# Kernel optimization log

Measured on AMD Instinct MI355X. Metric: run time of the kernel, lower is better.

## Reference

```python
import jax, jax.numpy as jnp
import numpy as np

N = 32768   # nodes
E = 32768   # edges
ND, ED, GD = 12, 5, 11
H = 64
T = 4
STEPS = 3


def setup_inputs() -> dict:
    key = jax.random.key(0)
    ks = jax.random.split(key, 24)
    s = 0.05
    p = lambda k, sh: (jax.random.normal(k, sh) * s).astype(jnp.float32)
    return dict(
        x=jax.random.normal(ks[0], (N, ND), jnp.float32),
        edge_index=jax.random.randint(ks[1], (2, E), 0, N, jnp.int64),
        edge_attr=jax.random.uniform(ks[2], (E, ED), jnp.float32),
        u=jax.random.normal(ks[3], (1, GD), jnp.float32),
        Wp=p(ks[4], (H, ND + GD)), bp=p(ks[5], (H,)),
        We1=p(ks[6], (H, ED)), be1=p(ks[7], (H,)),
        We2=p(ks[8], (H * H, H)), be2=p(ks[9], (H * H,)),
        root=p(ks[10], (H, H)), conv_b=p(ks[11], (H,)),
        Wih=p(ks[12], (3 * H, H)), bih=p(ks[13], (3 * H,)),
        Whh=p(ks[14], (3 * H, H)), bhh=p(ks[15], (3 * H,)),
        Wd1=p(ks[16], (H, 2 * H + ED)), bd1=p(ks[17], (H,)),
        Wd2=p(ks[18], (H // 2, H)), bd2=p(ks[19], (H // 2,)),
        Wd3=p(ks[20], (T, H // 2)), bd3=p(ks[21], (T,)),
    )


def _forward(x, edge_index, edge_attr, u,
             Wp, bp, We1, be1, We2, be2, root, conv_b,
             Wih, bih, Whh, bhh, Wd1, bd1, Wd2, bd2, Wd3, bd3):
    n = x.shape[0]
    e = edge_attr.shape[0]
    src, dst = edge_index[0], edge_index[1]

    # input projection with broadcast global features (batch=None path)
    u_node = jnp.broadcast_to(u, (n, u.shape[-1]))
    h = jnp.tanh(jnp.concatenate([x, u_node], axis=-1) @ Wp.T + bp)

    # edge MLP -> per-edge (H,H) weight matrices; edge_attr is loop-invariant
    ew = jax.nn.relu(edge_attr @ We1.T + be1) @ We2.T + be2   # (E, H*H)
    ew = ew.reshape(e, H, H)                                   # (E, H, H)

    # mean-aggregation denominators (clamped to 1 like scatter-mean)
    counts = jnp.clip(jax.ops.segment_sum(jnp.ones((e,), h.dtype), dst, num_segments=n), 1.0)

    for _ in range(STEPS):
        # NNConv: gather src features, per-edge matmul, scatter-mean into dst
        msg = jnp.einsum('eh,eho->eo', h[src], ew)             # (E, H)
        agg = jax.ops.segment_sum(msg, dst, num_segments=n) / counts[:, None]
        m = jax.nn.relu(agg + h @ root + conv_b)               # dropout off (eval)
        # GRUCell (torch gate order: r, z, n)
        gi = m @ Wih.T + bih
        gh = h @ Whh.T + bhh
        r = jax.nn.sigmoid(gi[:, :H] + gh[:, :H])
        z = jax.nn.sigmoid(gi[:, H:2 * H] + gh[:, H:2 * H])
        ng = jnp.tanh(gi[:, 2 * H:] + r * gh[:, 2 * H:])
        h = (1.0 - z) * ng + z * h

    # per-edge decoder
    e_in = jnp.concatenate([h[src], h[dst], edge_attr], axis=-1)
    d = jax.nn.relu(e_in @ Wd1.T + bd1)
    d = jax.nn.relu(d @ Wd2.T + bd2)
    return d @ Wd3.T + bd3                                     # (E, T)


def reference(x, edge_index, edge_attr, u,
              Wp, bp, We1, be1, We2, be2, root, conv_b,
              Wih, bih, Whh, bhh, Wd1, bd1, Wd2, bd2, Wd3, bd3):
    return _forward(x, edge_index, edge_attr, u,
                    Wp, bp, We1, be1, We2, be2, root, conv_b,
                    Wih, bih, Whh, bhh, Wd1, bd1, Wd2, bd2, Wd3, bd3)
```

## Files before the change

kernel.cpp:

```cpp
#include <hip/hip_runtime.h>
#include <hip/hip_bf16.h>
#include <stdint.h>


#define N_NODES 32768
#define N_EDGES 32768
#define STEPS 3

typedef __attribute__((ext_vector_type(8))) short short8;
typedef __attribute__((ext_vector_type(4))) float float4v;

__device__ __forceinline__ float bf2f(unsigned short u) {
    union { unsigned int i; float f; } v; v.i = ((unsigned int)u) << 16; return v.f;
}
__device__ __forceinline__ unsigned short f2bf(float f) {
    union { float f; unsigned int i; } v; v.f = f;
    unsigned int x = v.i;
    return (unsigned short)((x + 0x7fffu + ((x >> 16) & 1u)) >> 16);
}

__device__ __forceinline__ void gload_lds16(const void* g, void* l) {
    __builtin_amdgcn_global_load_lds(
        (__attribute__((address_space(1))) void*)g,
        (__attribute__((address_space(3))) void*)l, 16, 0, 0);
}

__global__ __launch_bounds__(256) void k_setup(
    const float* __restrict__ root, const float* __restrict__ Wih,
    const float* __restrict__ Whh,
    const float* __restrict__ We2, const float* __restrict__ be2,
    const float* __restrict__ Wd1, const float* __restrict__ bd1,
    const float* __restrict__ Wd2,
    const float* __restrict__ x, const float* __restrict__ u,
    const float* __restrict__ Wp, const float* __restrict__ bp,
    const float* __restrict__ ea, const float* __restrict__ We1,
    const float* __restrict__ be1,
    unsigned short* __restrict__ rootTf, unsigned short* __restrict__ wcombf,
    unsigned short* __restrict__ w2tf,
    unsigned short* __restrict__ wd1f, unsigned short* __restrict__ wd2f,
    unsigned short* __restrict__ hb,
    unsigned short* __restrict__ hidT, float* __restrict__ cnts)
{
    int b = blockIdx.x, tid = threadIdx.x;
    if (b < 144) {
        int i = b * 256 + tid;
        if (i < 4096) {
            int j = i & 7, lane = (i >> 3) & 63, g = i >> 9;
            int kb = g >> 2, nf = g & 3;
            int o = nf * 16 + (lane & 15);
            int k = kb * 32 + (lane >> 4) * 8 + j;
            rootTf[i] = f2bf(root[k * 64 + o]);
        } else if (i < 4096 + 32768) {
            int t = i - 4096;
            int j = t & 7, lane = (t >> 3) & 63, g = t >> 9;
            int kb = g >> 4, nf = g & 15;
            int cp = nf * 16 + (lane & 15);
            int k = kb * 32 + (lane >> 4) * 8 + j;
            float v;
            if (cp < 128)      v = (k < 64) ? Wih[cp * 64 + k] : Whh[cp * 64 + (k - 64)];
            else if (cp < 192) v = (k < 64) ? Wih[cp * 64 + k] : 0.f;
            else               v = (k < 64) ? 0.f : Whh[(cp - 64) * 64 + (k - 64)];
            wcombf[t] = f2bf(v);
        }
    } else if (b < 1184) {
        int t = (b - 144) * 256 + tid;
        if (t < 65 * 4096) {
            int kk = t >> 12, r = t & 4095;
            int j = r & 7, lane = (r >> 3) & 63, g = r >> 9;
            int half = g >> 2, nf = g & 3;
            int o = nf * 16 + (lane & 15);
            int hh = half * 32 + (lane >> 4) * 8 + j;
            float v = (kk < 64) ? We2[((size_t)(hh * 64 + o)) * 64 + kk]
                                : be2[(size_t)hh * 64 + o];
            w2tf[t] = f2bf(v);
        }
    } else if (b < 1232) {
        int i = (b - 1184) * 256 + tid;
        if (i < 10240) {
            int j = i & 7, lane = (i >> 3) & 63, g = i >> 9;
            int kb = g >> 2, nf = g & 3;
            int o = nf * 16 + (lane & 15);
            int k = kb * 32 + (lane >> 4) * 8 + j;
            float v = (k < 133) ? Wd1[(size_t)o * 133 + k] : (k == 133 ? bd1[o] : 0.f);
            wd1f[i] = f2bf(v);
        } else if (i < 10240 + 2048) {
            int t = i - 10240;
            int j = t & 7, lane = (t >> 3) & 63, g = t >> 9;
            int kb = g >> 1, nf = g & 1;
            int o = nf * 16 + (lane & 15);
            int k = kb * 32 + (lane >> 4) * 8 + j;
            wd2f[t] = f2bf(Wd2[(size_t)o * 64 + k]);
        }
    } else if (b < 9424) {
        int idx = (b - 1232) * 256 + tid;
        int n = idx >> 6, j = idx & 63;
        const float* wr = Wp + j * 23;
        const float* xr = x + (size_t)n * 12;
        float s = bp[j];
#pragma unroll
        for (int i = 0; i < 12; i++) s += xr[i] * wr[i];
#pragma unroll
        for (int i = 0; i < 11; i++) s += u[i] * wr[12 + i];
        hb[idx] = f2bf(tanhf(s));
    } else if (b < 17616) {
        int idx = (b - 9424) * 256 + tid;
        int el = idx & 63, j = (idx >> 6) & 63, eb = idx >> 12;
        int e = eb * 64 + el;
        float s = be1[j];
#pragma unroll
        for (int i = 0; i < 5; i++) s += ea[(size_t)e * 5 + i] * We1[j * 5 + i];
        hidT[(size_t)j * N_EDGES + e] = f2bf(s > 0.f ? s : 0.f);
    } else {
        int idx = (b - 17616) * 1024 + tid * 4;
        if (idx < 32768) {
            float4v z = {0.f, 0.f, 0.f, 0.f};
            *(float4v*)(cnts + idx) = z;
        }
    }
}

__global__ __launch_bounds__(256) void k_counts(
    const int* __restrict__ ei, float* __restrict__ counts)
{
    int i = blockIdx.x * 256 + threadIdx.x;
    if (i < N_EDGES) atomicAdd(&counts[ei[N_EDGES + i]], 1.0f);
}

__global__ __launch_bounds__(1024) void k_scan(
    const float* __restrict__ cnts, int* __restrict__ off, int* __restrict__ woff)
{
    __shared__ int part[1024];
    int t = threadIdx.x;
    int loc[32];
    int s = 0;
#pragma unroll
    for (int i = 0; i < 32; i++) { loc[i] = s; s += (int)cnts[t * 32 + i]; }
    part[t] = s;
    __syncthreads();
    for (int d = 1; d < 1024; d <<= 1) {
        int y = (t >= d) ? part[t - d] : 0;
        __syncthreads();
        part[t] += y;
        __syncthreads();
    }
    int pre = (t == 0) ? 0 : part[t - 1];
#pragma unroll
    for (int i = 0; i < 32; i++) {
        off[t * 32 + i] = pre + loc[i];
        woff[t * 32 + i] = pre + loc[i];
    }
    if (t == 1023) off[32768] = part[1023];
}

__global__ __launch_bounds__(256) void k_scatter(
    const int* __restrict__ ei, int* __restrict__ woff, int* __restrict__ eorder)
{
    int e = blockIdx.x * 256 + threadIdx.x;
    if (e < N_EDGES) {
        int d = ei[N_EDGES + e];
        int slot = atomicAdd(&woff[d], 1);
        eorder[slot] = e;
    }
}

__global__ __launch_bounds__(512, 2) void k_msg_fused(
    const unsigned short* __restrict__ hidT,
    const unsigned short* __restrict__ hb,
    const unsigned short* __restrict__ w2tf,
    const int* __restrict__ ei,
    float* __restrict__ msgbuf)
{
    __shared__ __attribute__((aligned(16))) unsigned char smem[81920];
    unsigned short* stg = (unsigned short*)smem;
    unsigned short* hvl = (unsigned short*)(smem + 65536);
    float* red = (float*)smem;

    int tid = threadIdx.x, w = tid >> 6, lane = tid & 63;
    int l15 = lane & 15, quad = lane >> 4;
    int kg = w & 3, eg = w >> 2;
    int ebase = blockIdx.x * 128;
    int n_w = 16 + (kg == 3 ? 1 : 0);

#pragma unroll
    for (int i = 0; i < 8; i++) {
        int row = w * 8 + i;
        unsigned int v = *((const unsigned int*)(hidT + (size_t)row * N_EDGES + ebase) + lane);
        *((unsigned int*)hvl + row * 64 + lane) = v;
    }
    short8 afr[4][2];
#pragma unroll
    for (int t = 0; t < 4; t++) {
        int src = ei[ebase + eg * 64 + t * 16 + l15];
#pragma unroll
        for (int hh = 0; hh < 2; hh++)
            afr[t][hh] = *(const short8*)(hb + (size_t)src * 64 + hh * 32 + quad * 8);
    }

    auto stage = [&](int r, int db) {
        const unsigned short* g = w2tf + (size_t)(kg * 16 + r) * 4096;
        unsigned short* d = stg + (kg * 2 + db) * 4096;
#pragma unroll
        for (int c = 0; c < 4; c++) {
            int ch = eg * 4 + c;
            gload_lds16(g + ch * 512 + lane * 8, d + ch * 512);
        }
    };

    stage(0, 0);
    stage(1, 1);
    asm volatile("s_waitcnt lgkmcnt(0)" ::: "memory");
    __builtin_amdgcn_s_barrier();

    float4v acc[4][4] = {};
    for (int r = 0; r <= 16; r++) {
        int db = r & 1;
        if (r >= n_w - 1) { asm volatile("s_waitcnt vmcnt(0)" ::: "memory"); }
        else              { asm volatile("s_waitcnt vmcnt(4)" ::: "memory"); }
        __builtin_amdgcn_s_barrier();

        bool act = (r < n_w);
        short8 bfr[2][4];
        unsigned long long hu[4] = {0ull, 0ull, 0ull, 0ull};
        bool bias = (r == 16);
        if (act) {
            const unsigned short* bb = stg + (kg * 2 + db) * 4096;
#pragma unroll
            for (int hh = 0; hh < 2; hh++)
#pragma unroll
                for (int nf = 0; nf < 4; nf++)
                    bfr[hh][nf] = *(const short8*)(bb + (hh * 4 + nf) * 512 + lane * 8);
            if (!bias) {
#pragma unroll
                for (int t = 0; t < 4; t++)
                    hu[t] = *(const unsigned long long*)(hvl + (kg * 16 + r) * 128 + eg * 64 + t * 16 + quad * 4);
            }
        }
        asm volatile("s_waitcnt lgkmcnt(0)" ::: "memory");
        __builtin_amdgcn_s_barrier();
        if (r + 2 < n_w) stage(r + 2, db);

        if (act) {
#pragma unroll
            for (int t = 0; t < 4; t++) {
                float4v T[4];
#pragma unroll
                for (int nf = 0; nf < 4; nf++) {
                    float4v z = {0.f, 0.f, 0.f, 0.f};
                    T[nf] = __builtin_amdgcn_mfma_f32_16x16x32_bf16(afr[t][0], bfr[0][nf], z, 0, 0, 0);
                }
#pragma unroll
                for (int nf = 0; nf < 4; nf++)
                    T[nf] = __builtin_amdgcn_mfma_f32_16x16x32_bf16(afr[t][1], bfr[1][nf], T[nf], 0, 0, 0);
#pragma unroll
                for (int rr = 0; rr < 4; rr++) {
                    float hvv = bias ? 1.0f : bf2f((unsigned short)(hu[t] >> (16 * rr)));
#pragma unroll
                    for (int nf = 0; nf < 4; nf++)
                        acc[t][nf][rr] += hvv * T[nf][rr];
                }
            }
        }
    }

    int row_w = tid >> 2, kq = tid & 3;
#pragma unroll
    for (int nf = 0; nf < 4; nf++) {
        __syncthreads();
#pragma unroll
        for (int t = 0; t < 4; t++)
#pragma unroll
            for (int rr = 0; rr < 4; rr++)
                red[kg * 2304 + (eg * 64 + t * 16 + quad * 4 + rr) * 18 + l15] = acc[t][nf][rr];
        __syncthreads();
        float4v s = {0.f, 0.f, 0.f, 0.f};
#pragma unroll
        for (int g2 = 0; g2 < 4; g2++) {
            const float* rp = red + g2 * 2304 + row_w * 18 + kq * 4;
#pragma unroll
            for (int j = 0; j < 4; j++) s[j] += rp[j];
        }
        *(float4v*)(msgbuf + (size_t)(ebase + row_w) * 64 + nf * 16 + kq * 4) = s;
    }
}

__global__ __launch_bounds__(256) void k_node(
    const unsigned short* __restrict__ hb_in,
    const unsigned short* __restrict__ rootTf,
    const unsigned short* __restrict__ wcombf,
    const float* __restrict__ msgbuf, const int* __restrict__ off,
    const int* __restrict__ eorder,
    const float* __restrict__ counts,
    const float* __restrict__ conv_b,
    const float* __restrict__ bih, const float* __restrict__ bhh,
    unsigned short* __restrict__ hb_out)
{
    __shared__ unsigned short m_lds[64 * 72];
    __shared__ float aggl[64 * 68];
    int tid = threadIdx.x, w = tid >> 6, lane = tid & 63;
    int l15 = lane & 15, quad = lane >> 4;
    int node0 = blockIdx.x * 64;
    int row0 = w * 16;

    {
        int nl = tid >> 2, cg = tid & 3;
        int nn = node0 + nl;
        int s0 = off[nn], s1 = off[nn + 1];
        float acc[16] = {};
        for (int sl = s0; sl < s1; sl++) {
            int e = eorder[sl];
            const float* mr = msgbuf + (size_t)e * 64 + cg * 16;
#pragma unroll
            for (int q = 0; q < 4; q++) {
                float4v v = *(const float4v*)(mr + 4 * q);
#pragma unroll
                for (int j = 0; j < 4; j++) acc[4 * q + j] += v[j];
            }
        }
#pragma unroll
        for (int k = 0; k < 16; k++) aggl[nl * 68 + cg * 16 + k] = acc[k];
    }
    __syncthreads();

    float4v acc1[4] = {};
    {
        short8 a1[2];
#pragma unroll
        for (int kb = 0; kb < 2; kb++)
            a1[kb] = *(const short8*)(hb_in + (size_t)(node0 + row0 + l15) * 64 + kb * 32 + quad * 8);
#pragma unroll
        for (int kb = 0; kb < 2; kb++)
#pragma unroll
            for (int nf = 0; nf < 4; nf++) {
                short8 b = *(const short8*)(rootTf + (size_t)((kb * 4 + nf) * 64 + lane) * 8);
                acc1[nf] = __builtin_amdgcn_mfma_f32_16x16x32_bf16(a1[kb], b, acc1[nf], 0, 0, 0);
            }
    }
#pragma unroll
    for (int rr = 0; rr < 4; rr++) {
        int nl = row0 + quad * 4 + rr;
        float cnt = counts[node0 + nl]; if (cnt < 1.f) cnt = 1.f;
        float rcp = 1.f / cnt;
#pragma unroll
        for (int nf = 0; nf < 4; nf++) {
            int c = nf * 16 + l15;
            float av = aggl[nl * 68 + c];
            float mv = av * rcp + acc1[nf][rr] + conv_b[c];
            m_lds[nl * 72 + c] = f2bf(mv > 0.f ? mv : 0.f);
        }
    }
    __syncthreads();

    float4v acc2[16] = {};
#pragma unroll
    for (int kb = 0; kb < 4; kb++) {
        short8 a2;
        if (kb < 2)
            a2 = *(const short8*)(m_lds + (row0 + l15) * 72 + kb * 32 + quad * 8);
        else
            a2 = *(const short8*)(hb_in + (size_t)(node0 + row0 + l15) * 64 + (kb - 2) * 32 + quad * 8);
#pragma unroll
        for (int nf = 0; nf < 16; nf++) {
            short8 b = *(const short8*)(wcombf + (size_t)((kb * 16 + nf) * 64 + lane) * 8);
            acc2[nf] = __builtin_amdgcn_mfma_f32_16x16x32_bf16(a2, b, acc2[nf], 0, 0, 0);
        }
    }

#pragma unroll
    for (int nf0 = 0; nf0 < 4; nf0++) {
        int c = nf0 * 16 + l15;
        float br = bih[c] + bhh[c];
        float bz = bih[64 + c] + bhh[64 + c];
        float bni = bih[128 + c], bnh = bhh[128 + c];
#pragma unroll
        for (int rr = 0; rr < 4; rr++) {
            int node = node0 + row0 + quad * 4 + rr;
            float gr = 1.f / (1.f + __expf(-(acc2[nf0][rr] + br)));
            float gz = 1.f / (1.f + __expf(-(acc2[nf0 + 4][rr] + bz)));
            float ng = tanhf(acc2[nf0 + 8][rr] + bni + gr * (acc2[nf0 + 12][rr] + bnh));
            float ho = bf2f(hb_in[(size_t)node * 64 + c]);
            float hn = (1.f - gz) * ng + gz * ho;
            hb_out[(size_t)node * 64 + c] = f2bf(hn);
        }
    }
}

__global__ __launch_bounds__(256) void k_decoder(
    const unsigned short* __restrict__ hb, const int* __restrict__ ei,
    const float* __restrict__ ea,
    const unsigned short* __restrict__ wd1f, const unsigned short* __restrict__ wd2f,
    const float* __restrict__ bd2,
    const float* __restrict__ Wd3, const float* __restrict__ bd3,
    float* __restrict__ out)
{
    __shared__ unsigned short d1f[4][1024];
    __shared__ float d2s[4][16 * 33];
    int tid = threadIdx.x, w = tid >> 6, lane = tid & 63;
    int l15 = lane & 15, quad = lane >> 4;
    int ebase = blockIdx.x * 64 + w * 16;
    int e = ebase + l15;
    int src = ei[e], dst = ei[N_EDGES + e];

    short8 a[5];
#pragma unroll
    for (int kb = 0; kb < 2; kb++) {
        a[kb]     = *(const short8*)(hb + (size_t)src * 64 + kb * 32 + quad * 8);
        a[2 + kb] = *(const short8*)(hb + (size_t)dst * 64 + kb * 32 + quad * 8);
    }
    {
        union { short8 v; unsigned short u[8]; } tea;
#pragma unroll
        for (int j = 0; j < 8; j++) {
            float vv = 0.f;
            if (quad == 0) vv = (j < 5) ? ea[(size_t)e * 5 + j] : (j == 5 ? 1.f : 0.f);
            tea.u[j] = f2bf(vv);
        }
        a[4] = tea.v;
    }

    float4v acc1[4] = {};
#pragma unroll
    for (int kb = 0; kb < 5; kb++)
#pragma unroll
        for (int nf = 0; nf < 4; nf++) {
            short8 b = *(const short8*)(wd1f + (size_t)((kb * 4 + nf) * 64 + lane) * 8);
            acc1[nf] = __builtin_amdgcn_mfma_f32_16x16x32_bf16(a[kb], b, acc1[nf], 0, 0, 0);
        }
#pragma unroll
    for (int nf = 0; nf < 4; nf++) {
        int kbp = nf >> 1;
        int lanep_hi = ((nf & 1) * 2 + (l15 >> 3)) * 16;
        int jp = l15 & 7;
#pragma unroll
        for (int r = 0; r < 4; r++) {
            float v = acc1[nf][r];
            d1f[w][kbp * 512 + (lanep_hi + quad * 4 + r) * 8 + jp] = f2bf(v > 0.f ? v : 0.f);
        }
    }
    float4v acc2[2] = {};
#pragma unroll
    for (int kb = 0; kb < 2; kb++) {
        short8 a2 = *(const short8*)(&d1f[w][kb * 512 + lane * 8]);
#pragma unroll
        for (int nf = 0; nf < 2; nf++) {
            short8 b = *(const short8*)(wd2f + (size_t)((kb * 2 + nf) * 64 + lane) * 8);
            acc2[nf] = __builtin_amdgcn_mfma_f32_16x16x32_bf16(a2, b, acc2[nf], 0, 0, 0);
        }
    }
#pragma unroll
    for (int nf = 0; nf < 2; nf++) {
        int c = nf * 16 + l15;
        float bias = bd2[c];
#pragma unroll
        for (int r = 0; r < 4; r++) {
            float v = acc2[nf][r] + bias;
            d2s[w][(quad * 4 + r) * 33 + c] = v > 0.f ? v : 0.f;
        }
    }
    {
        int e_l = lane >> 2, t = lane & 3;
        float s = bd3[t];
        const float* w3 = Wd3 + t * 32;
        const float* dr = &d2s[w][e_l * 33];
#pragma unroll
        for (int k = 0; k < 32; k++) s += w3[k] * dr[k];
        out[(size_t)(ebase + e_l) * 4 + t] = s;
    }
}

extern "C" void kernel_launch(void* const* d_in, const int* in_sizes, int n_in,
                              void* d_out, int out_size, void* d_ws, size_t ws_size,
                              hipStream_t stream)
{
    const float* x      = (const float*)d_in[0];
    const int*   ei     = (const int*)d_in[1];
    const float* ea     = (const float*)d_in[2];
    const float* u      = (const float*)d_in[3];
    const float* Wp     = (const float*)d_in[4];
    const float* bp     = (const float*)d_in[5];
    const float* We1    = (const float*)d_in[6];
    const float* be1    = (const float*)d_in[7];
    const float* We2    = (const float*)d_in[8];
    const float* be2    = (const float*)d_in[9];
    const float* root   = (const float*)d_in[10];
    const float* conv_b = (const float*)d_in[11];
    const float* Wih    = (const float*)d_in[12];
    const float* bih    = (const float*)d_in[13];
    const float* Whh    = (const float*)d_in[14];
    const float* bhh    = (const float*)d_in[15];
    const float* Wd1    = (const float*)d_in[16];
    const float* bd1    = (const float*)d_in[17];
    const float* Wd2    = (const float*)d_in[18];
    const float* bd2    = (const float*)d_in[19];
    const float* Wd3    = (const float*)d_in[20];
    const float* bd3    = (const float*)d_in[21];
    float* out = (float*)d_out;

    char* ws = (char*)d_ws;
    size_t off_b = 0;
    auto take = [&](size_t bytes) -> char* {
        char* p = ws + off_b; off_b = (off_b + bytes + 255) & ~(size_t)255; return p;
    };
    unsigned short* hb     = (unsigned short*)take((size_t)N_NODES * 64 * 2);
    unsigned short* hidT   = (unsigned short*)take((size_t)N_EDGES * 64 * 2);
    float*          msgbuf = (float*)take((size_t)N_EDGES * 64 * 4);
    float*          cnts   = (float*)take((size_t)N_NODES * 4);
    int*            off    = (int*)take((size_t)(N_NODES + 1) * 4);
    int*            woff   = (int*)take((size_t)N_NODES * 4);
    int*            eorder = (int*)take((size_t)N_EDGES * 4);
    unsigned short* w2tf   = (unsigned short*)take((size_t)66 * 4096 * 2);
    unsigned short* rootTf = (unsigned short*)take((size_t)4096 * 2);
    unsigned short* wcombf = (unsigned short*)take((size_t)32768 * 2);
    unsigned short* wd1f   = (unsigned short*)take((size_t)10240 * 2);
    unsigned short* wd2f   = (unsigned short*)take((size_t)2048 * 2);
    (void)ws_size;

    k_setup<<<17648, 256, 0, stream>>>(root, Wih, Whh, We2, be2, Wd1, bd1, Wd2,
                                       x, u, Wp, bp, ea, We1, be1,
                                       rootTf, wcombf, w2tf, wd1f, wd2f,
                                       hb, hidT, cnts);
    k_counts<<<128, 256, 0, stream>>>(ei, cnts);
    k_scan<<<1, 1024, 0, stream>>>(cnts, off, woff);
    k_scatter<<<128, 256, 0, stream>>>(ei, woff, eorder);

    for (int s = 0; s < STEPS; s++) {
        k_msg_fused<<<N_EDGES / 128, 512, 0, stream>>>(hidT, hb, w2tf, ei, msgbuf);
        k_node<<<N_NODES / 64, 256, 0, stream>>>(hb, rootTf, wcombf, msgbuf, off,
                                                 eorder, cnts, conv_b, bih, bhh, hb);
    }
    k_decoder<<<N_EDGES / 64, 256, 0, stream>>>(hb, ei, ea, wd1f, wd2f, bd2,
                                                Wd3, bd3, out);
}
```

Measured before the change: 271.8 us.

## Repartition msg kernel warps by output columns to drop per-step block barriers

Result: faster. 261.9 us (-3.6%).

```diff
diff --git a/kernel.cpp b/kernel.cpp
--- a/kernel.cpp
+++ b/kernel.cpp
@@ -170,116 +170,114 @@
     const int* __restrict__ ei,
     float* __restrict__ msgbuf)
 {
-    __shared__ __attribute__((aligned(16))) unsigned char smem[81920];
+    __shared__ __attribute__((aligned(16))) unsigned char smem[98304];
     unsigned short* stg = (unsigned short*)smem;
     unsigned short* hvl = (unsigned short*)(smem + 65536);
     float* red = (float*)smem;
 
     int tid = threadIdx.x, w = tid >> 6, lane = tid & 63;
     int l15 = lane & 15, quad = lane >> 4;
-    int kg = w & 3, eg = w >> 2;
+    int kg = w & 3, nfh = w >> 2;
     int ebase = blockIdx.x * 128;
     int n_w = 16 + (kg == 3 ? 1 : 0);
 
-#pragma unroll
-    for (int i = 0; i < 8; i++) {
-        int row = w * 8 + i;
-        unsigned int v = *((const unsigned int*)(hidT + (size_t)row * N_EDGES + ebase) + lane);
-        *((unsigned int*)hvl + row * 64 + lane) = v;
-    }
-    short8 afr[4][2];
-#pragma unroll
-    for (int t = 0; t < 4; t++) {
-        int src = ei[ebase + eg * 64 + t * 16 + l15];
+    unsigned short* hvp = hvl + w * 2048;
+#pragma unroll
+    for (int r2 = 0; r2 < 16; r2++) {
+        unsigned int v = *((const unsigned int*)(hidT + (size_t)(kg * 16 + r2) * N_EDGES + ebase) + lane);
+        *((unsigned int*)hvp + r2 * 64 + lane) = v;
+    }
+    short8 afr[8][2];
+#pragma unroll
+    for (int t = 0; t < 8; t++) {
+        int src = ei[ebase + t * 16 + l15];
 #pragma unroll
         for (int hh = 0; hh < 2; hh++)
             afr[t][hh] = *(const short8*)(hb + (size_t)src * 64 + hh * 32 + quad * 8);
     }
 
+    unsigned short* wbuf = stg + w * 4096;
     auto stage = [&](int r, int db) {
         const unsigned short* g = w2tf + (size_t)(kg * 16 + r) * 4096;
-        unsigned short* d = stg + (kg * 2 + db) * 4096;
+        unsigned short* d = wbuf + db * 2048;
 #pragma unroll
         for (int c = 0; c < 4; c++) {
-            int ch = eg * 4 + c;
-            gload_lds16(g + ch * 512 + lane * 8, d + ch * 512);
+            int hh = c >> 1, j = c & 1;
+            gload_lds16(g + (hh * 4 + nfh * 2 + j) * 512 + lane * 8, d + c * 512);
         }
     };
 
     stage(0, 0);
     stage(1, 1);
     asm volatile("s_waitcnt lgkmcnt(0)" ::: "memory");
-    __builtin_amdgcn_s_barrier();
-
-    float4v acc[4][4] = {};
-    for (int r = 0; r <= 16; r++) {
+
+    float4v acc[8][2] = {};
+    for (int r = 0; r < n_w; r++) {
         int db = r & 1;
-        if (r >= n_w - 1) { asm volatile("s_waitcnt vmcnt(0)" ::: "memory"); }
-        else              { asm volatile("s_waitcnt vmcnt(4)" ::: "memory"); }
-        __builtin_amdgcn_s_barrier();
-
-        bool act = (r < n_w);
-        short8 bfr[2][4];
-        unsigned long long hu[4] = {0ull, 0ull, 0ull, 0ull};
+        if (r < n_w - 1) { asm volatile("s_waitcnt vmcnt(4)" ::: "memory"); }
+        else             { asm volatile("s_waitcnt vmcnt(0)" ::: "memory"); }
+
         bool bias = (r == 16);
-        if (act) {
-            const unsigned short* bb = stg + (kg * 2 + db) * 4096;
-#pragma unroll
-            for (int hh = 0; hh < 2; hh++)
-#pragma unroll
-                for (int nf = 0; nf < 4; nf++)
-                    bfr[hh][nf] = *(const short8*)(bb + (hh * 4 + nf) * 512 + lane * 8);
-            if (!bias) {
-#pragma unroll
-                for (int t = 0; t < 4; t++)
-                    hu[t] = *(const unsigned long long*)(hvl + (kg * 16 + r) * 128 + eg * 64 + t * 16 + quad * 4);
+        short8 bfr[2][2];
+        const unsigned short* bb = wbuf + db * 2048;
+#pragma unroll
+        for (int hh = 0; hh < 2; hh++)
+#pragma unroll
+            for (int j = 0; j < 2; j++)
+                bfr[hh][j] = *(const short8*)(bb + (hh * 2 + j) * 512 + lane * 8);
+
+        unsigned long long hu[8] = {};
+        if (!bias) {
+#pragma unroll
+            for (int t = 0; t < 8; t++)
+                hu[t] = *(const unsigned long long*)(hvp + r * 128 + t * 16 + quad * 4);
+        }
+
+        asm volatile("s_waitcnt lgkmcnt(0)" ::: "memory");
+        if (r + 2 < n_w) stage(r + 2, db);
+
+#pragma unroll
+        for (int t = 0; t < 8; t++) {
+            float4v z = {0.f, 0.f, 0.f, 0.f};
+            float4v T0 = __builtin_amdgcn_mfma_f32_16x16x32_bf16(afr[t][0], bfr[0][0], z, 0, 0, 0);
+            T0 = __builtin_amdgcn_mfma_f32_16x16x32_bf16(afr[t][1], bfr[1][0], T0, 0, 0, 0);
+            float4v T1 = __builtin_amdgcn_mfma_f32_16x16x32_bf16(afr[t][0], bfr[0][1], z, 0, 0, 0);
+            T1 = __builtin_amdgcn_mfma_f32_16x16x32_bf16(afr[t][1], bfr[1][1], T1, 0, 0, 0);
+#pragma unroll
+            for (int rr = 0; rr < 4; rr++) {
+                float hvv = bias ? 1.0f : bf2f((unsigned short)(hu[t] >> (16 * rr)));
+                acc[t][0][rr] += hvv * T0[rr];
+                acc[t][1][rr] += hvv * T1[rr];
             }
         }
-        asm volatile("s_waitcnt lgkmcnt(0)" ::: "memory");
-        __builtin_amdgcn_s_barrier();
-        if (r + 2 < n_w) stage(r + 2, db);
-
-        if (act) {
-#pragma unroll
-            for (int t = 0; t < 4; t++) {
-                float4v T[4];
-#pragma unroll
-                for (int nf = 0; nf < 4; nf++) {
-                    float4v z = {0.f, 0.f, 0.f, 0.f};
-                    T[nf] = __builtin_amdgcn_mfma_f32_16x16x32_bf16(afr[t][0], bfr[0][nf], z, 0, 0, 0);
-                }
-#pragma unroll
-                for (int nf = 0; nf < 4; nf++)
-                    T[nf] = __builtin_amdgcn_mfma_f32_16x16x32_bf16(afr[t][1], bfr[1][nf], T[nf], 0, 0, 0);
-#pragma unroll
-                for (int rr = 0; rr < 4; rr++) {
-                    float hvv = bias ? 1.0f : bf2f((unsigned short)(hu[t] >> (16 * rr)));
-#pragma unroll
-                    for (int nf = 0; nf < 4; nf++)
-                        acc[t][nf][rr] += hvv * T[nf][rr];
-                }
-            }
-        }
-    }
-
-    int row_w = tid >> 2, kq = tid & 3;
-#pragma unroll
-    for (int nf = 0; nf < 4; nf++) {
+    }
+
+    int row_r = tid >> 2, cq = tid & 3;
+#pragma unroll
+    for (int nf2 = 0; nf2 < 2; nf2++) {
         __syncthreads();
 #pragma unroll
-        for (int t = 0; t < 4; t++)
+        for (int t = 0; t < 8; t++)
 #pragma unroll
             for (int rr = 0; rr < 4; rr++)
-                red[kg * 2304 + (eg * 64 + t * 16 + quad * 4 + rr) * 18 + l15] = acc[t][nf][rr];
+                red[kg * 4352 + (t * 16 + quad * 4 + rr) * 34 + nfh * 16 + l15] = acc[t][nf2][rr];
         __syncthreads();
-        float4v s = {0.f, 0.f, 0.f, 0.f};
+        float s[8];
+#pragma unroll
+        for (int i = 0; i < 8; i++) s[i] = 0.f;
 #pragma unroll
         for (int g2 = 0; g2 < 4; g2++) {
-            const float* rp = red + g2 * 2304 + row_w * 18 + kq * 4;
-#pragma unroll
-            for (int j = 0; j < 4; j++) s[j] += rp[j];
-        }
-        *(float4v*)(msgbuf + (size_t)(ebase + row_w) * 64 + nf * 16 + kq * 4) = s;
+            const float* rp = red + g2 * 4352 + row_r * 34 + cq * 8;
+#pragma unroll
+            for (int i = 0; i < 8; i++) s[i] += rp[i];
+        }
+        int c34 = cq * 8;
+        int gcol = ((c34 >> 4) * 2 + nf2) * 16 + (c34 & 15);
+        float* op = msgbuf + (size_t)(ebase + row_r) * 64 + gcol;
+        float4v v0 = { s[0], s[1], s[2], s[3] };
+        float4v v1 = { s[4], s[5], s[6], s[7] };
+        *(float4v*)(op) = v0;
+        *(float4v*)(op + 4) = v1;
     }
 }
 
```
